# Kernel optimization log

Hardware: AMD Instinct MI355X
Metric: run time of the kernel (lower is better)

## Reference

```python
import jax, jax.numpy as jnp
import numpy as np

E = 768      # image_embedding
H = 12       # attention_head
DH = E // H  # head_dim = 64; NOTE: seq_len MUST equal DH for this module's math
S = DH       # seq_len = 64
B = 1024
HID = 3072   # hidden_layer
EPS = 1e-6


def setup_inputs() -> dict:
    key = jax.random.key(0)
    ks = jax.random.split(key, 12)
    sd = 0.02
    return {
        "image": jax.random.normal(ks[0], (B, S, E), dtype=jnp.float32),
        # single shared LayerNorm (used before both attention and MLP)
        "ln_g": jnp.ones((E,), dtype=jnp.float32),
        "ln_b": jnp.zeros((E,), dtype=jnp.float32),
        # Q/K/V linears, stored as [in, out]
        "Wq": jax.random.normal(ks[1], (E, E), dtype=jnp.float32) * sd,
        "bq": jnp.zeros((E,), dtype=jnp.float32),
        "Wk": jax.random.normal(ks[2], (E, E), dtype=jnp.float32) * sd,
        "bk": jnp.zeros((E,), dtype=jnp.float32),
        "Wv": jax.random.normal(ks[3], (E, E), dtype=jnp.float32) * sd,
        "bv": jnp.zeros((E,), dtype=jnp.float32),
        # MLP
        "W1": jax.random.normal(ks[4], (E, HID), dtype=jnp.float32) * sd,
        "b1": jnp.zeros((HID,), dtype=jnp.float32),
        "W2": jax.random.normal(ks[5], (HID, E), dtype=jnp.float32) * sd,
        "b2": jnp.zeros((E,), dtype=jnp.float32),
    }


def _layernorm(x, g, b):
    mu = jnp.mean(x, axis=-1, keepdims=True)
    var = jnp.mean(jnp.square(x - mu), axis=-1, keepdims=True)
    return (x - mu) * jax.lax.rsqrt(var + EPS) * g + b


def _heads(x):  # [B,S,E] -> [B,H,S,DH]
    b, s, _ = x.shape
    return x.reshape(b, s, H, DH).transpose(0, 2, 1, 3)


def reference(image, ln_g, ln_b, Wq, bq, Wk, bk, Wv, bv, W1, b1, W2, b2):
    b, s, e = image.shape
    # --- attention branch (pre-norm, shared LN) ---
    hn = _layernorm(image, ln_g, ln_b)
    q = _heads(hn @ Wq + bq)  # [B,H,S,DH]
    k = _heads(hn @ Wk + bk)
    v = _heads(hn @ Wv + bv)
    # NOTE: original scales by sqrt(embed_dim), NOT sqrt(head_dim)
    score = jax.nn.softmax(jnp.einsum("bhsd,bhtd->bhst", q, k) / jnp.sqrt(jnp.float32(e)), axis=-1)
    # NOTE: original computes value @ score (not score @ value): [B,H,S,DH]@[B,H,S,S]
    # requires DH == S; then reshapes [B,H,S,S] directly to [B,S,E]
    attn = jnp.einsum("bhsd,bhdt->bhst", v, score).reshape(b, s, e)
    x = image + attn
    # --- MLP branch (same shared LN; dropout=0 in eval) ---
    hn2 = _layernorm(x, ln_g, ln_b)
    mlp = jax.nn.gelu(hn2 @ W1 + b1, approximate=False) @ W2 + b2
    return x + mlp
```

## Files before the change

### kernel.cpp

```cpp
#include <hip/hip_runtime.h>
#include <hip/hip_bf16.h>
#include <cstdint>
#include <cstddef>


typedef __bf16 bf16;
typedef __bf16 bf16x8 __attribute__((ext_vector_type(8)));
typedef __bf16 bf16x4 __attribute__((ext_vector_type(4)));
typedef float  f32x4  __attribute__((ext_vector_type(4)));

#define LDS_ASYNC16(lds, g)                                                     \
  __builtin_amdgcn_global_load_lds(                                             \
      (const __attribute__((address_space(1))) void*)(g),                       \
      (__attribute__((address_space(3))) void*)(lds), 16, 0, 0)

#define NROWS 65536
#define E_DIM 768
#define HID_DIM 3072
#define HEADS 12
#define QKV_N 2304

__global__ __launch_bounds__(256) void transpose_cast(
    const float* __restrict__ in, bf16* __restrict__ out, int K, int N) {
  __shared__ float tile[32][33];
  int tx = threadIdx.x & 31, ty = threadIdx.x >> 5;
  int n0 = blockIdx.x * 32, k0 = blockIdx.y * 32;
#pragma unroll
  for (int i = 0; i < 4; ++i)
    tile[ty + 8 * i][tx] = in[(size_t)(k0 + ty + 8 * i) * N + n0 + tx];
  __syncthreads();
#pragma unroll
  for (int i = 0; i < 4; ++i)
    out[(size_t)(n0 + ty + 8 * i) * K + k0 + tx] = (bf16)tile[tx][ty + 8 * i];
}

__global__ __launch_bounds__(256) void pack_bias(
    const float* __restrict__ bq, const float* __restrict__ bk,
    const float* __restrict__ bv, float* __restrict__ o) {
  int i = blockIdx.x * 256 + threadIdx.x;
  const float* src = i < 768 ? bq : (i < 1536 ? bk : bv);
  o[i] = src[i & 767];
}

__global__ __launch_bounds__(256) void ln_kernel(
    const float* __restrict__ x, const float* __restrict__ gam,
    const float* __restrict__ bet, bf16* __restrict__ out) {
  int row  = blockIdx.x * 4 + (threadIdx.x >> 6);
  int lane = threadIdx.x & 63;
  const float4* xr = (const float4*)(x + (size_t)row * E_DIM);
  float4 v[3];
  float s = 0.f, ss = 0.f;
#pragma unroll
  for (int i = 0; i < 3; ++i) {
    v[i] = xr[lane + 64 * i];
    s  += v[i].x + v[i].y + v[i].z + v[i].w;
    ss += v[i].x * v[i].x + v[i].y * v[i].y + v[i].z * v[i].z + v[i].w * v[i].w;
  }
#pragma unroll
  for (int m = 1; m < 64; m <<= 1) {
    s  += __shfl_xor(s, m);
    ss += __shfl_xor(ss, m);
  }
  float mean = s * (1.f / 768.f);
  float var  = ss * (1.f / 768.f) - mean * mean;
  float rstd = rsqrtf(var + 1e-6f);
  bf16x4* o = (bf16x4*)(out + (size_t)row * E_DIM);
#pragma unroll
  for (int i = 0; i < 3; ++i) {
    float4 g4 = ((const float4*)gam)[lane + 64 * i];
    float4 b4 = ((const float4*)bet)[lane + 64 * i];
    bf16x4 r;
    r[0] = (bf16)((v[i].x - mean) * rstd * g4.x + b4.x);
    r[1] = (bf16)((v[i].y - mean) * rstd * g4.y + b4.y);
    r[2] = (bf16)((v[i].z - mean) * rstd * g4.z + b4.z);
    r[3] = (bf16)((v[i].w - mean) * rstd * g4.w + b4.w);
    o[lane + 64 * i] = r;
  }
}

__global__ __launch_bounds__(256) void attn_kernel(
    const bf16* __restrict__ qkv, const float* __restrict__ image,
    float* __restrict__ xout) {
  __shared__ __align__(16) bf16 qs[64 * 72];
  __shared__ __align__(16) bf16 ks[64 * 72];
  __shared__ __align__(16) bf16 vs[64 * 72];
  __shared__ __align__(16) bf16 pT[64 * 72];

  const int t = threadIdx.x, w = t >> 6, lane = t & 63;
  const int quad = lane >> 4, l15 = lane & 15;
  const int h = blockIdx.x % HEADS, b = blockIdx.x / HEADS;

  const bf16* base = qkv + (size_t)(b * 64) * QKV_N + h * 64;
#pragma unroll
  for (int i = 0; i < 2; ++i) {
    int slot = i * 256 + t;
    int row = slot >> 3, c = (slot & 7) * 8;
    size_t go = (size_t)row * QKV_N + c;
    *(bf16x8*)&qs[row * 72 + c] = *(const bf16x8*)&base[go];
    *(bf16x8*)&ks[row * 72 + c] = *(const bf16x8*)&base[go + 768];
    *(bf16x8*)&vs[row * 72 + c] = *(const bf16x8*)&base[go + 1536];
  }
  __syncthreads();

  f32x4 sc[4] = {};
#pragma unroll
  for (int kk = 0; kk < 2; ++kk) {
    bf16x8 af = *(const bf16x8*)&qs[(w * 16 + l15) * 72 + kk * 32 + quad * 8];
#pragma unroll
    for (int ni = 0; ni < 4; ++ni) {
      bf16x8 bfr = *(const bf16x8*)&ks[(ni * 16 + l15) * 72 + kk * 32 + quad * 8];
      sc[ni] = __builtin_amdgcn_mfma_f32_16x16x32_bf16(af, bfr, sc[ni], 0, 0, 0);
    }
  }

  const float inv_sqrt_e = 0.03608439182435161f;
#pragma unroll
  for (int r = 0; r < 4; ++r) {
    float s0 = sc[0][r] * inv_sqrt_e, s1 = sc[1][r] * inv_sqrt_e;
    float s2 = sc[2][r] * inv_sqrt_e, s3 = sc[3][r] * inv_sqrt_e;
    float mx = fmaxf(fmaxf(s0, s1), fmaxf(s2, s3));
    mx = fmaxf(mx, __shfl_xor(mx, 1));
    mx = fmaxf(mx, __shfl_xor(mx, 2));
    mx = fmaxf(mx, __shfl_xor(mx, 4));
    mx = fmaxf(mx, __shfl_xor(mx, 8));
    float e0 = __expf(s0 - mx), e1 = __expf(s1 - mx);
    float e2 = __expf(s2 - mx), e3 = __expf(s3 - mx);
    float sm = e0 + e1 + e2 + e3;
    sm += __shfl_xor(sm, 1);
    sm += __shfl_xor(sm, 2);
    sm += __shfl_xor(sm, 4);
    sm += __shfl_xor(sm, 8);
    float inv = 1.f / sm;
    sc[0][r] = e0 * inv; sc[1][r] = e1 * inv;
    sc[2][r] = e2 * inv; sc[3][r] = e3 * inv;
  }

#pragma unroll
  for (int ni = 0; ni < 4; ++ni) {
    int tc = ni * 16 + l15;
#pragma unroll
    for (int r = 0; r < 4; ++r) {
      int s = w * 16 + quad * 4 + r;
      pT[tc * 72 + s] = (bf16)sc[ni][r];
    }
  }
  __syncthreads();

  f32x4 ao[4] = {};
#pragma unroll
  for (int kk = 0; kk < 2; ++kk) {
    bf16x8 af = *(const bf16x8*)&vs[(w * 16 + l15) * 72 + kk * 32 + quad * 8];
#pragma unroll
    for (int ni = 0; ni < 4; ++ni) {
      bf16x8 bfr = *(const bf16x8*)&pT[(ni * 16 + l15) * 72 + kk * 32 + quad * 8];
      ao[ni] = __builtin_amdgcn_mfma_f32_16x16x32_bf16(af, bfr, ao[ni], 0, 0, 0);
    }
  }

  size_t base_o = (size_t)b * 49152 + (size_t)h * 4096;
#pragma unroll
  for (int ni = 0; ni < 4; ++ni) {
    int tc = ni * 16 + l15;
#pragma unroll
    for (int r = 0; r < 4; ++r) {
      int s = w * 16 + quad * 4 + r;
      size_t off = base_o + (size_t)s * 64 + tc;
      xout[off] = image[off] + ao[ni][r];
    }
  }
}

__device__ inline float gelu_f(float x) {
  float u = x * (0.7978845608028654f + 0.0356774081f * x * x);
  float e = __expf(2.f * u);
  float th = 1.f - 2.f / (e + 1.f);
  return 0.5f * x * (1.f + th);
}

__device__ __forceinline__ f32x4 mfma8(bf16x8 a, bf16x8 b, f32x4 c) {
  return __builtin_amdgcn_mfma_f32_16x16x32_bf16(a, b, c, 0, 0, 0);
}

#define LDF(P, OFF) (*(const bf16x8*)((P) + (OFF)))

template <int EPI>
__global__ __launch_bounds__(512) void gemm256(
    const bf16* __restrict__ A, const bf16* __restrict__ B,
    const float* __restrict__ bias, bf16* __restrict__ outb, float* outf,
    const float* resid, int M, int N, int K) {
  __shared__ __align__(16) char lds[131072];
  const int t = threadIdx.x;
  const int wq = t >> 6, lane = t & 63;
  const int quad = lane >> 4, l15 = lane & 15;
  const int wm = wq >> 2, wn = wq & 3;

  const int Ntile = (int)gridDim.x;
  const int fid = (int)blockIdx.y * Ntile + (int)blockIdx.x;
  const int xcd = fid & 7, j = fid >> 3;
  const int bm = xcd * 32 + j / Ntile;
  const int bn = j % Ntile;

  const int NT = K >> 6;
  const size_t rowK = (size_t)K;

  const int tr = t >> 3, ts = t & 7;
  const bf16* aSrc = A + ((size_t)bm * 256 + tr) * rowK + ((ts ^ (tr & 7)) << 3);
  const bf16* bSrc = B + ((size_t)bn * 256 + tr) * rowK + ((ts ^ (tr & 7)) << 3);

  char* ldsA = (char*)lds;
  char* ldsB = (char*)lds + 65536;
  const int stDst = wq * 1024;

#define STAGE_H(LB, BUFP, H, SRC, KT)                                           \
  do {                                                                          \
    LDS_ASYNC16((LB) + (BUFP) * 32768 + ((H) * 128 + 0) * 128 + stDst,          \
                (SRC) + (size_t)((H) * 128 + 0) * rowK + (size_t)(KT) * 64);    \
    LDS_ASYNC16((LB) + (BUFP) * 32768 + ((H) * 128 + 64) * 128 + stDst,         \
                (SRC) + (size_t)((H) * 128 + 64) * rowK + (size_t)(KT) * 64);   \
  } while (0)

  STAGE_H(ldsA, 0, 0, aSrc, 0);
  STAGE_H(ldsA, 0, 1, aSrc, 0);
  STAGE_H(ldsB, 0, 0, bSrc, 0);
  STAGE_H(ldsB, 0, 1, bSrc, 0);
  STAGE_H(ldsA, 1, 0, aSrc, 1);
  asm volatile("s_waitcnt vmcnt(2)" ::: "memory");
  __builtin_amdgcn_s_barrier();

  const int sx = l15 & 7;
  const int c0 = (quad ^ sx) << 4;
  const int c1 = ((4 + quad) ^ sx) << 4;
  const int arow = (wm * 64 + l15) * 128;
  const int brow = (wn * 64 + l15) * 128;

  f32x4 acc[8][4] = {};

  for (int g = 0; g < NT; ++g) {
    const int bufp = g & 1, nx = bufp ^ 1;
    const char* Ab = ldsA + bufp * 32768;
    const char* Bb = ldsB + bufp * 32768;

    if (g + 1 < NT) {
      STAGE_H(ldsA, nx, 1, aSrc, g + 1);
      STAGE_H(ldsB, nx, 0, bSrc, g + 1);
      STAGE_H(ldsB, nx, 1, bSrc, g + 1);
    }

    bf16x8 bReg[4][2], aF0[4][2], aF1[4][2];
#pragma unroll
    for (int ni = 0; ni < 4; ++ni) {
      bReg[ni][0] = LDF(Bb, brow + ni * 2048 + c0);
      bReg[ni][1] = LDF(Bb, brow + ni * 2048 + c1);
    }
#pragma unroll
    for (int mi = 0; mi < 4; ++mi) {
      aF0[mi][0] = LDF(Ab, arow + mi * 2048 + c0);
      aF0[mi][1] = LDF(Ab, arow + mi * 2048 + c1);
    }
#pragma unroll
    for (int mi = 0; mi < 4; ++mi) {
      aF1[mi][0] = LDF(Ab, arow + 16384 + mi * 2048 + c0);
      aF1[mi][1] = LDF(Ab, arow + 16384 + mi * 2048 + c1);
    }

    __builtin_amdgcn_s_setprio(1);
#pragma unroll
    for (int mi = 0; mi < 4; ++mi)
#pragma unroll
      for (int ni = 0; ni < 4; ++ni) {
        acc[mi][ni] = mfma8(aF0[mi][0], bReg[ni][0], acc[mi][ni]);
        acc[mi][ni] = mfma8(aF0[mi][1], bReg[ni][1], acc[mi][ni]);
      }
    __builtin_amdgcn_s_setprio(0);

    asm volatile("s_waitcnt lgkmcnt(0)" ::: "memory");
    __builtin_amdgcn_s_barrier();
    if (g + 2 < NT) STAGE_H(ldsA, bufp, 0, aSrc, g + 2);

    __builtin_amdgcn_s_setprio(1);
#pragma unroll
    for (int mi = 0; mi < 4; ++mi)
#pragma unroll
      for (int ni = 0; ni < 4; ++ni) {
        acc[4 + mi][ni] = mfma8(aF1[mi][0], bReg[ni][0], acc[4 + mi][ni]);
        acc[4 + mi][ni] = mfma8(aF1[mi][1], bReg[ni][1], acc[4 + mi][ni]);
      }
    __builtin_amdgcn_s_setprio(0);

    asm volatile("s_waitcnt lgkmcnt(0)" ::: "memory");
    if (g < NT - 2)
      asm volatile("s_waitcnt vmcnt(2)" ::: "memory");
    else if (g == NT - 2)
      asm volatile("s_waitcnt vmcnt(0)" ::: "memory");
    __builtin_amdgcn_s_barrier();
  }
#undef STAGE_H

  const int row0 = bm * 256 + wm * 64 + quad * 4;
  const int col0 = bn * 256 + wn * 64 + l15;
#pragma unroll
  for (int mi = 0; mi < 8; ++mi) {
    const int rbase = row0 + (mi >> 2) * 128 + (mi & 3) * 16;
#pragma unroll
    for (int ni = 0; ni < 4; ++ni) {
      const int col = col0 + ni * 16;
      const float bc = bias[col];
#pragma unroll
      for (int r = 0; r < 4; ++r) {
        const int row = rbase + r;
        const float v = acc[mi][ni][r] + bc;
        const size_t off = (size_t)row * N + col;
        if (EPI == 0)      outb[off] = (bf16)gelu_f(v);
        else if (EPI == 1) outf[off] = resid[off] + v;
        else               outb[off] = (bf16)v;
      }
    }
  }
}

extern "C" void kernel_launch(void* const* d_in, const int* in_sizes, int n_in,
                              void* d_out, int out_size, void* d_ws,
                              size_t ws_size, hipStream_t stream) {
  const float* image = (const float*)d_in[0];
  const float* ln_g  = (const float*)d_in[1];
  const float* ln_b  = (const float*)d_in[2];
  const float* Wq    = (const float*)d_in[3];
  const float* bq    = (const float*)d_in[4];
  const float* Wk    = (const float*)d_in[5];
  const float* bk    = (const float*)d_in[6];
  const float* Wv    = (const float*)d_in[7];
  const float* bv    = (const float*)d_in[8];
  const float* W1    = (const float*)d_in[9];
  const float* b1    = (const float*)d_in[10];
  const float* W2    = (const float*)d_in[11];
  const float* b2    = (const float*)d_in[12];
  float* out = (float*)d_out;

  char* ws = (char*)d_ws;
  bf16* hn   = (bf16*)ws;  ws += (size_t)NROWS * E_DIM * 2;
  bf16* h1   = (bf16*)ws;
  bf16* qkv  = (bf16*)ws;  ws += (size_t)NROWS * HID_DIM * 2;
  bf16* WqkvT = (bf16*)ws; ws += (size_t)QKV_N * E_DIM * 2;
  bf16* W1T  = (bf16*)ws;  ws += (size_t)E_DIM * HID_DIM * 2;
  bf16* W2T  = (bf16*)ws;  ws += (size_t)E_DIM * HID_DIM * 2;
  float* bqkv = (float*)ws; ws += QKV_N * 4;

  dim3 blk(256);
  dim3 blk512(512);
  transpose_cast<<<dim3(24, 24), blk, 0, stream>>>(Wq, WqkvT, 768, 768);
  transpose_cast<<<dim3(24, 24), blk, 0, stream>>>(Wk, WqkvT + 768 * 768, 768, 768);
  transpose_cast<<<dim3(24, 24), blk, 0, stream>>>(Wv, WqkvT + 2 * 768 * 768, 768, 768);
  transpose_cast<<<dim3(96, 24), blk, 0, stream>>>(W1, W1T, 768, 3072);
  transpose_cast<<<dim3(24, 96), blk, 0, stream>>>(W2, W2T, 3072, 768);
  pack_bias<<<dim3(9), blk, 0, stream>>>(bq, bk, bv, bqkv);

  ln_kernel<<<NROWS / 4, blk, 0, stream>>>(image, ln_g, ln_b, hn);
  gemm256<2><<<dim3(QKV_N / 256, NROWS / 256), blk512, 0, stream>>>(
      hn, WqkvT, bqkv, qkv, nullptr, nullptr, NROWS, QKV_N, E_DIM);
  attn_kernel<<<1024 * HEADS, blk, 0, stream>>>(qkv, image, out);
  ln_kernel<<<NROWS / 4, blk, 0, stream>>>(out, ln_g, ln_b, hn);
  gemm256<0><<<dim3(HID_DIM / 256, NROWS / 256), blk512, 0, stream>>>(
      hn, W1T, b1, h1, nullptr, nullptr, NROWS, HID_DIM, E_DIM);
  gemm256<1><<<dim3(E_DIM / 256, NROWS / 256), blk512, 0, stream>>>(
      h1, W2T, b2, nullptr, out, out, NROWS, E_DIM, HID_DIM);
}
```

Before: 1.583 ms.

## Make GEMM persistent over N tiles and overlap epilogue with next tile's MFMAs

Replaces the 2D tile grid with one block per 256-row M tile (256 blocks), each walking all N tiles in a single flattened K×N loop. The double-buffered staging pipeline keeps running across N-tile boundaries, and the previous tile's epilogue stores are issued while the next tile's first MFMAs run. This is meant to remove per-tile prologue and pipeline drain and to hide store latency. The cost is that parallelism is fixed at 256 blocks, which may underfill the GPU. Register pressure also rises because the epilogue sits inside the main loop.

```diff
diff --git a/kernel.cpp b/kernel.cpp
--- a/kernel.cpp
+++ b/kernel.cpp
@@ -184,46 +184,44 @@
 #define LDF(P, OFF) (*(const bf16x8*)((P) + (OFF)))
 
 template <int EPI>
-__global__ __launch_bounds__(512) void gemm256(
+__global__ __launch_bounds__(512) void gemm256p(
     const bf16* __restrict__ A, const bf16* __restrict__ B,
     const float* __restrict__ bias, bf16* __restrict__ outb, float* outf,
-    const float* resid, int M, int N, int K) {
+    const float* resid, int N, int K) {
   __shared__ __align__(16) char lds[131072];
   const int t = threadIdx.x;
   const int wq = t >> 6, lane = t & 63;
   const int quad = lane >> 4, l15 = lane & 15;
   const int wm = wq >> 2, wn = wq & 3;
 
-  const int Ntile = (int)gridDim.x;
-  const int fid = (int)blockIdx.y * Ntile + (int)blockIdx.x;
-  const int xcd = fid & 7, j = fid >> 3;
-  const int bm = xcd * 32 + j / Ntile;
-  const int bn = j % Ntile;
-
   const int NT = K >> 6;
+  const int NB = N >> 8;
+  const int U = NB * NT;
   const size_t rowK = (size_t)K;
+  const int bm = (int)blockIdx.x;
 
   const int tr = t >> 3, ts = t & 7;
-  const bf16* aSrc = A + ((size_t)bm * 256 + tr) * rowK + ((ts ^ (tr & 7)) << 3);
-  const bf16* bSrc = B + ((size_t)bn * 256 + tr) * rowK + ((ts ^ (tr & 7)) << 3);
+  const size_t srcOff = (size_t)tr * rowK + ((ts ^ (tr & 7)) << 3);
+  const bf16* aP = A + (size_t)bm * 256 * rowK + srcOff;
+  const bf16* bP = B + srcOff;
 
   char* ldsA = (char*)lds;
   char* ldsB = (char*)lds + 65536;
   const int stDst = wq * 1024;
 
-#define STAGE_H(LB, BUFP, H, SRC, KT)                                           \
+#define STAGE_H(LB, BUFP, H, SRC)                                               \
   do {                                                                          \
     LDS_ASYNC16((LB) + (BUFP) * 32768 + ((H) * 128 + 0) * 128 + stDst,          \
-                (SRC) + (size_t)((H) * 128 + 0) * rowK + (size_t)(KT) * 64);    \
+                (SRC) + (size_t)((H) * 128 + 0) * rowK);                        \
     LDS_ASYNC16((LB) + (BUFP) * 32768 + ((H) * 128 + 64) * 128 + stDst,         \
-                (SRC) + (size_t)((H) * 128 + 64) * rowK + (size_t)(KT) * 64);   \
+                (SRC) + (size_t)((H) * 128 + 64) * rowK);                       \
   } while (0)
 
-  STAGE_H(ldsA, 0, 0, aSrc, 0);
-  STAGE_H(ldsA, 0, 1, aSrc, 0);
-  STAGE_H(ldsB, 0, 0, bSrc, 0);
-  STAGE_H(ldsB, 0, 1, bSrc, 0);
-  STAGE_H(ldsA, 1, 0, aSrc, 1);
+  STAGE_H(ldsA, 0, 0, aP);
+  STAGE_H(ldsA, 0, 1, aP);
+  STAGE_H(ldsB, 0, 0, bP);
+  STAGE_H(ldsB, 0, 1, bP);
+  STAGE_H(ldsA, 1, 0, aP + 64);
   asm volatile("s_waitcnt vmcnt(2)" ::: "memory");
   __builtin_amdgcn_s_barrier();
 
@@ -232,18 +230,51 @@
   const int c1 = ((4 + quad) ^ sx) << 4;
   const int arow = (wm * 64 + l15) * 128;
   const int brow = (wn * 64 + l15) * 128;
+  const int row0 = bm * 256 + wm * 64 + quad * 4;
 
   f32x4 acc[8][4] = {};
 
-  for (int g = 0; g < NT; ++g) {
-    const int bufp = g & 1, nx = bufp ^ 1;
+#define EPI_WRITE(BND)                                                          \
+  do {                                                                          \
+    const int col0e = (BND) * 256 + wn * 64 + l15;                              \
+    _Pragma("unroll")                                                           \
+    for (int mi = 0; mi < 8; ++mi) {                                            \
+      const int rbase = row0 + (mi >> 2) * 128 + (mi & 3) * 16;                 \
+      _Pragma("unroll")                                                         \
+      for (int ni = 0; ni < 4; ++ni) {                                          \
+        const int col = col0e + ni * 16;                                        \
+        const float bc = bias[col];                                             \
+        _Pragma("unroll")                                                       \
+        for (int r = 0; r < 4; ++r) {                                           \
+          const int row = rbase + r;                                            \
+          const float v = acc[mi][ni][r] + bc;                                  \
+          const size_t off = (size_t)row * N + col;                             \
+          if (EPI == 0)      outb[off] = (bf16)gelu_f(v);                       \
+          else if (EPI == 1) outf[off] = resid[off] + v;                        \
+          else               outb[off] = (bf16)v;                               \
+          acc[mi][ni][r] = 0.f;                                                 \
+        }                                                                       \
+      }                                                                         \
+    }                                                                           \
+  } while (0)
+
+  int kt = 0, bn = 0;
+  int kt1 = 1, bn1 = 0;
+  size_t bOff1 = 0;
+
+  for (int u = 0; u < U; ++u) {
+    const int bufp = u & 1, nx = bufp ^ 1;
     const char* Ab = ldsA + bufp * 32768;
     const char* Bb = ldsB + bufp * 32768;
 
-    if (g + 1 < NT) {
-      STAGE_H(ldsA, nx, 1, aSrc, g + 1);
-      STAGE_H(ldsB, nx, 0, bSrc, g + 1);
-      STAGE_H(ldsB, nx, 1, bSrc, g + 1);
+    int kt2 = kt1 + 1, bn2 = bn1;
+    size_t bOff2 = bOff1;
+    if (kt2 == NT) { kt2 = 0; bn2 = bn1 + 1; bOff2 += (size_t)256 * rowK; }
+
+    if (u + 1 < U) {
+      STAGE_H(ldsA, nx, 1, aP + kt1 * 64);
+      STAGE_H(ldsB, nx, 0, bP + bOff1 + kt1 * 64);
+      STAGE_H(ldsB, nx, 1, bP + bOff1 + kt1 * 64);
     }
 
     bf16x8 bReg[4][2], aF0[4][2], aF1[4][2];
@@ -262,6 +293,8 @@
       aF1[mi][0] = LDF(Ab, arow + 16384 + mi * 2048 + c0);
       aF1[mi][1] = LDF(Ab, arow + 16384 + mi * 2048 + c1);
     }
+
+    if (kt == 0 && u > 0) EPI_WRITE(bn - 1);
 
     __builtin_amdgcn_s_setprio(1);
 #pragma unroll
@@ -275,7 +308,7 @@
 
     asm volatile("s_waitcnt lgkmcnt(0)" ::: "memory");
     __builtin_amdgcn_s_barrier();
-    if (g + 2 < NT) STAGE_H(ldsA, bufp, 0, aSrc, g + 2);
+    if (u + 2 < U) STAGE_H(ldsA, bufp, 0, aP + kt2 * 64);
 
     __builtin_amdgcn_s_setprio(1);
 #pragma unroll
@@ -288,34 +321,19 @@
     __builtin_amdgcn_s_setprio(0);
 
     asm volatile("s_waitcnt lgkmcnt(0)" ::: "memory");
-    if (g < NT - 2)
+    if (u < U - 2)
       asm volatile("s_waitcnt vmcnt(2)" ::: "memory");
-    else if (g == NT - 2)
+    else if (u == U - 2)
       asm volatile("s_waitcnt vmcnt(0)" ::: "memory");
     __builtin_amdgcn_s_barrier();
+
+    kt = kt1; bn = bn1;
+    kt1 = kt2; bn1 = bn2; bOff1 = bOff2;
   }
 #undef STAGE_H
 
-  const int row0 = bm * 256 + wm * 64 + quad * 4;
-  const int col0 = bn * 256 + wn * 64 + l15;
-#pragma unroll
-  for (int mi = 0; mi < 8; ++mi) {
-    const int rbase = row0 + (mi >> 2) * 128 + (mi & 3) * 16;
-#pragma unroll
-    for (int ni = 0; ni < 4; ++ni) {
-      const int col = col0 + ni * 16;
-      const float bc = bias[col];
-#pragma unroll
-      for (int r = 0; r < 4; ++r) {
-        const int row = rbase + r;
-        const float v = acc[mi][ni][r] + bc;
-        const size_t off = (size_t)row * N + col;
-        if (EPI == 0)      outb[off] = (bf16)gelu_f(v);
-        else if (EPI == 1) outf[off] = resid[off] + v;
-        else               outb[off] = (bf16)v;
-      }
-    }
-  }
+  EPI_WRITE(NB - 1);
+#undef EPI_WRITE
 }
 
 extern "C" void kernel_launch(void* const* d_in, const int* in_sizes, int n_in,
@@ -355,12 +373,12 @@
   pack_bias<<<dim3(9), blk, 0, stream>>>(bq, bk, bv, bqkv);
 
   ln_kernel<<<NROWS / 4, blk, 0, stream>>>(image, ln_g, ln_b, hn);
-  gemm256<2><<<dim3(QKV_N / 256, NROWS / 256), blk512, 0, stream>>>(
-      hn, WqkvT, bqkv, qkv, nullptr, nullptr, NROWS, QKV_N, E_DIM);
+  gemm256p<2><<<dim3(256), blk512, 0, stream>>>(
+      hn, WqkvT, bqkv, qkv, nullptr, nullptr, QKV_N, E_DIM);
   attn_kernel<<<1024 * HEADS, blk, 0, stream>>>(qkv, image, out);
   ln_kernel<<<NROWS / 4, blk, 0, stream>>>(out, ln_g, ln_b, hn);
-  gemm256<0><<<dim3(HID_DIM / 256, NROWS / 256), blk512, 0, stream>>>(
-      hn, W1T, b1, h1, nullptr, nullptr, NROWS, HID_DIM, E_DIM);
-  gemm256<1><<<dim3(E_DIM / 256, NROWS / 256), blk512, 0, stream>>>(
-      h1, W2T, b2, nullptr, out, out, NROWS, E_DIM, HID_DIM);
-}
+  gemm256p<0><<<dim3(256), blk512, 0, stream>>>(
+      hn, W1T, b1, h1, nullptr, nullptr, HID_DIM, E_DIM);
+  gemm256p<1><<<dim3(256), blk512, 0, stream>>>(
+      h1, W2T, b2, nullptr, out, out, E_DIM, HID_DIM);
+}
```

Result: slower. 1.896 ms (+19.8%).
